# Optimization experiments

Hardware: AMD Instinct MI355X
Metric: run time of the kernel (lower is better)

Reference implementation:

```python
import jax, jax.numpy as jnp
import numpy as np

B, T, C = 2, 2048, 1024
H = 16
D = C // H  # head_dim = 64
SCALE = D ** -0.5


def setup_inputs() -> dict:
    key = jax.random.key(0)
    ks = jax.random.split(key, 5)
    s = 0.02
    return {
        "x": jax.random.normal(ks[0], (B, T, C), dtype=jnp.float32),
        "w_qkv": jax.random.normal(ks[1], (C, 3 * C), dtype=jnp.float32) * s,
        "b_qkv": jnp.zeros((3 * C,), dtype=jnp.float32),
        "w_proj": jax.random.normal(ks[2], (C, C), dtype=jnp.float32) * s,
        "b_proj": jnp.zeros((C,), dtype=jnp.float32),
    }


def reference(x, w_qkv, b_qkv, w_proj, b_proj):
    Bx, Tx, Cx = x.shape
    qkv = x @ w_qkv + b_qkv                      # [B,T,3C]
    q, k, v = jnp.split(qkv, 3, axis=-1)
    # [B,T,C] -> [B,H,T,D]
    q = q.reshape(Bx, Tx, H, D).transpose(0, 2, 1, 3)
    k = k.reshape(Bx, Tx, H, D).transpose(0, 2, 1, 3)
    v = v.reshape(Bx, Tx, H, D).transpose(0, 2, 1, 3)
    attn = jnp.einsum('bhqd,bhkd->bhqk', q, k) * SCALE
    causal = jnp.tril(jnp.ones((Tx, Tx), dtype=bool))
    attn = jnp.where(causal[None, None], attn, -jnp.inf)
    attn = jax.nn.softmax(attn, axis=-1)
    out = jnp.einsum('bhqk,bhkd->bhqd', attn, v)  # [B,H,T,D]
    out = out.transpose(0, 2, 1, 3).reshape(Bx, Tx, Cx)
    return out @ w_proj + b_proj
```

## Files before the change

kernel.cpp:

```cpp
#include <hip/hip_runtime.h>
#include <hip/hip_bf16.h>
#include <math.h>

#define T_SEQ 2048
#define NHEAD 16
#define HDIM  64
#define CDIM  1024
#define KDIM  1024
#define SCALE_L2E 0.1803368801111204f

typedef __attribute__((ext_vector_type(8))) short bf16x8;
typedef __attribute__((ext_vector_type(4))) float f32x4;
typedef __attribute__((ext_vector_type(16))) float f32x16;
typedef __attribute__((ext_vector_type(8))) unsigned short u16x8;
typedef __attribute__((ext_vector_type(4))) unsigned int u32x4;

__device__ __forceinline__ unsigned short f2bf(float f) {
    unsigned int u = __builtin_bit_cast(unsigned int, f);
    u += 0x7fffu + ((u >> 16) & 1u);
    return (unsigned short)(u >> 16);
}
__device__ __forceinline__ unsigned int cvt_pk_bf16(float lo, float hi_) {
    unsigned int r;
    asm("v_cvt_pk_bf16_f32 %0, %1, %2" : "=v"(r) : "v"(lo), "v"(hi_));
    return r;
}
__device__ __forceinline__ void pl32swap(unsigned int &a, unsigned int &b) {
    asm("v_permlane32_swap_b32 %0, %1" : "+v"(a), "+v"(b));
}
__device__ __forceinline__ void gld16(const unsigned short* g, unsigned short* l) {
    __builtin_amdgcn_global_load_lds(
        (const __attribute__((address_space(1))) unsigned int*)g,
        (__attribute__((address_space(3))) unsigned int*)l,
        16, 0, 0);
}

__global__ __launch_bounds__(256) void prep_x(const float* __restrict__ x,
                                              unsigned short* __restrict__ Xb) {
    size_t i = ((size_t)blockIdx.x * 256 + threadIdx.x) * 8;
    float4 a = *(const float4*)(x + i);
    float4 b = *(const float4*)(x + i + 4);
    u32x4 o;
    o[0] = cvt_pk_bf16(a.x, a.y);
    o[1] = cvt_pk_bf16(a.z, a.w);
    o[2] = cvt_pk_bf16(b.x, b.y);
    o[3] = cvt_pk_bf16(b.z, b.w);
    *(u32x4*)(Xb + i) = o;
}

template<int NC>
__global__ __launch_bounds__(256) void prep_w(const float* __restrict__ W,
                                              unsigned short* __restrict__ Wt) {
    __shared__ unsigned short Ls[64][72];
    const int n0 = blockIdx.x * 64, k0 = blockIdx.y * 64;
    const int t = threadIdx.x;
    {
        int kr = t >> 2, nc = (t & 3) * 16;
        #pragma unroll
        for (int j = 0; j < 4; j++) {
            float4 v = *(const float4*)(W + (size_t)(k0 + kr) * NC + n0 + nc + j * 4);
            Ls[nc + j*4 + 0][kr] = f2bf(v.x);
            Ls[nc + j*4 + 1][kr] = f2bf(v.y);
            Ls[nc + j*4 + 2][kr] = f2bf(v.z);
            Ls[nc + j*4 + 3][kr] = f2bf(v.w);
        }
    }
    __syncthreads();
    {
        int nr = t >> 2, kc = (t & 3) * 16;
        u16x8 o0 = *(const u16x8*)&Ls[nr][kc];
        u16x8 o1 = *(const u16x8*)&Ls[nr][kc + 8];
        *(u16x8*)(Wt + (size_t)(n0 + nr) * KDIM + k0 + kc)     = o0;
        *(u16x8*)(Wt + (size_t)(n0 + nr) * KDIM + k0 + kc + 8) = o1;
    }
}

template<int NC, int EPI>
__global__ __launch_bounds__(256) void gemm_k(
    const unsigned short* __restrict__ A, const unsigned short* __restrict__ Wt,
    const float* __restrict__ bias, float* __restrict__ Of,
    unsigned short* __restrict__ Qb, unsigned short* __restrict__ Kb,
    unsigned short* __restrict__ Vt)
{
    __shared__ unsigned short As[128 * 64];
    __shared__ unsigned short Bs[128 * 64];

    const int tid  = threadIdx.x;
    const int lane = tid & 63;
    const int wid  = tid >> 6;
    const int m0 = blockIdx.x * 128;
    const int n0 = blockIdx.y * 128;
    const int wm = (wid >> 1) * 64;
    const int wn = (wid & 1) * 64;
    const int rl = lane & 15;

    const int r8 = lane >> 3, s8 = lane & 7;
    const int swzs = (s8 ^ r8) * 8;

    f32x4 acc[4][4] = {};

    for (int k0 = 0; k0 < KDIM; k0 += 64) {
        #pragma unroll
        for (int c = 0; c < 4; c++) {
            int row = (wid << 5) + (c << 3) + r8;
            gld16(A  + (size_t)(m0 + row) * KDIM + k0 + swzs, &As[(size_t)((wid<<5)+(c<<3)) * 64]);
            gld16(Wt + (size_t)(n0 + row) * KDIM + k0 + swzs, &Bs[(size_t)((wid<<5)+(c<<3)) * 64]);
        }
        __syncthreads();
        #pragma unroll
        for (int kc = 0; kc < 2; kc++) {
            const int sb = kc * 4 + (lane >> 4);
            bf16x8 af[4], bfr[4];
            #pragma unroll
            for (int f = 0; f < 4; f++) {
                int sw = (sb ^ (rl & 7)) * 8;
                af[f]  = *(const bf16x8*)&As[(wm + f*16 + rl) * 64 + sw];
                bfr[f] = *(const bf16x8*)&Bs[(wn + f*16 + rl) * 64 + sw];
            }
            __builtin_amdgcn_s_setprio(1);
            #pragma unroll
            for (int i = 0; i < 4; i++)
                #pragma unroll
                for (int j = 0; j < 4; j++)
                    acc[i][j] = __builtin_amdgcn_mfma_f32_16x16x32_bf16(af[i], bfr[j], acc[i][j], 0, 0, 0);
            __builtin_amdgcn_s_setprio(0);
        }
        __syncthreads();
    }

    #pragma unroll
    for (int j = 0; j < 4; j++) {
        int gn = n0 + wn + j*16 + rl;
        float bv = bias[gn];
        #pragma unroll
        for (int i = 0; i < 4; i++) {
            int gm0 = m0 + wm + i*16 + (lane >> 4) * 4;
            #pragma unroll
            for (int r = 0; r < 4; r++) {
                float v = acc[i][j][r] + bv;
                int gm = gm0 + r;
                if (EPI == 0) {
                    int which = gn >> 10;
                    int cw = gn & 1023;
                    int h = cw >> 6, d = cw & 63;
                    int b = gm >> 11, t = gm & 2047;
                    size_t bh = (size_t)(b * NHEAD + h);
                    if (which == 0)      Qb[(bh * T_SEQ + t) * HDIM + d] = f2bf(v * SCALE_L2E);
                    else if (which == 1) Kb[(bh * T_SEQ + t) * HDIM + d] = f2bf(v);
                    else                 Vt[(bh * HDIM + d) * T_SEQ + t] = f2bf(v);
                } else {
                    Of[(size_t)gm * NC + gn] = v;
                }
            }
        }
    }
}

__global__ __launch_bounds__(128, 4) void attn_k(
    const unsigned short* __restrict__ Qb, const unsigned short* __restrict__ Kb,
    const unsigned short* __restrict__ Vt, unsigned short* __restrict__ AO)
{
    __shared__ unsigned short sbuf[2 * 4096];

    const int tid  = threadIdx.x;
    const int lane = tid & 63;
    const int w    = tid >> 6;
    const int bh   = blockIdx.x;
    const int qt   = 63 - blockIdx.y;
    const int ql   = lane & 31;
    const int hi   = lane >> 5;
    const int qg   = (qt << 5) + ql;

    const unsigned short* Qp = Qb + (size_t)bh * T_SEQ * HDIM;
    const unsigned short* Kp = Kb + (size_t)bh * T_SEQ * HDIM;
    const unsigned short* Vp = Vt + (size_t)bh * HDIM * T_SEQ;

    unsigned short* kbuf = sbuf + w * 4096;
    const char* kbB = (const char*)kbuf;
    const char* vbB = (const char*)(kbuf + 2048);

    const int r8 = lane >> 3, s8 = lane & 7;
    const int r4 = lane >> 2, s4 = lane & 3;
    const unsigned short* kSrc = Kp + (size_t)r8 * HDIM + ((s8 ^ r8) << 3);
    const unsigned short* vSrc = Vp + (size_t)r4 * T_SEQ + ((s4 ^ (r4 & 3)) << 3);

    auto issue_tile = [&](int t) {
        #pragma unroll
        for (int c = 0; c < 4; c++)
            gld16(kSrc + ((size_t)t << 11) + (c << 9), kbuf + (c << 9));
        #pragma unroll
        for (int c = 0; c < 4; c++)
            gld16(vSrc + ((size_t)c << 15) + (t << 5), kbuf + 2048 + (c << 9));
    };

    bf16x8 qf[4];
    #pragma unroll
    for (int dc = 0; dc < 4; dc++)
        qf[dc] = *(const bf16x8*)(Qp + (size_t)qg * HDIM + dc*16 + hi*8);

    float m_run = -INFINITY, l_run = 0.f;
    f32x16 o0 = {}, o1 = {};

    if (w <= qt) {
        issue_tile(w);
        for (int t = w; t <= qt; t += 2) {
            asm volatile("s_waitcnt vmcnt(0)" ::: "memory");
            __builtin_amdgcn_sched_barrier(0);

            bf16x8 kf[4];
            #pragma unroll
            for (int dc = 0; dc < 4; dc++)
                kf[dc] = *(const bf16x8*)(kbB + ql*128 + (((dc << 1 | hi) ^ (ql & 7)) << 4));
            bf16x8 v00 = *(const bf16x8*)(vbB + ql*64        + (((0 | hi) ^ (ql & 3)) << 4));
            bf16x8 v01 = *(const bf16x8*)(vbB + ql*64        + (((2 | hi) ^ (ql & 3)) << 4));
            bf16x8 v10 = *(const bf16x8*)(vbB + (32+ql)*64   + (((0 | hi) ^ (ql & 3)) << 4));
            bf16x8 v11 = *(const bf16x8*)(vbB + (32+ql)*64   + (((2 | hi) ^ (ql & 3)) << 4));
            asm volatile("s_waitcnt lgkmcnt(0)" ::: "memory");
            __builtin_amdgcn_sched_barrier(0);

            if (t + 2 <= qt) issue_tile(t + 2);

            f32x16 s = {};
            __builtin_amdgcn_s_setprio(1);
            #pragma unroll
            for (int dc = 0; dc < 4; dc++)
                s = __builtin_amdgcn_mfma_f32_32x32x16_bf16(kf[dc], qf[dc], s, 0, 0, 0);
            __builtin_amdgcn_s_setprio(0);

            float p[16];
            #pragma unroll
            for (int r = 0; r < 16; r++) p[r] = s[r];
            if (t == qt) {
                #pragma unroll
                for (int r = 0; r < 16; r++) {
                    int kv = (t << 5) + (r & 3) + 8 * (r >> 2) + 4 * hi;
                    p[r] = (kv > qg) ? -INFINITY : p[r];
                }
            }
            float tm = p[0];
            #pragma unroll
            for (int r = 1; r < 16; r++) tm = fmaxf(tm, p[r]);
            tm = fmaxf(tm, __shfl_xor(tm, 32));
            if (__any(tm > m_run + 11.5f)) {
                float mn = fmaxf(m_run, tm);
                float sf = exp2f(m_run - mn);
                m_run = mn;
                l_run *= sf;
                #pragma unroll
                for (int r = 0; r < 16; r++) { o0[r] *= sf; o1[r] *= sf; }
            }
            float rs = 0.f;
            #pragma unroll
            for (int r = 0; r < 16; r++) { p[r] = exp2f(p[r] - m_run); rs += p[r]; }
            rs += __shfl_xor(rs, 32);
            l_run += rs;

            unsigned int c[8];
            #pragma unroll
            for (int i = 0; i < 8; i++) c[i] = cvt_pk_bf16(p[2*i], p[2*i+1]);
            pl32swap(c[0], c[2]);  pl32swap(c[1], c[3]);
            pl32swap(c[4], c[6]);  pl32swap(c[5], c[7]);
            u32x4 b0 = {c[0], c[1], c[2], c[3]};
            u32x4 b1 = {c[4], c[5], c[6], c[7]};
            bf16x8 pf0 = __builtin_bit_cast(bf16x8, b0);
            bf16x8 pf1 = __builtin_bit_cast(bf16x8, b1);

            __builtin_amdgcn_s_setprio(1);
            o0 = __builtin_amdgcn_mfma_f32_32x32x16_bf16(v00, pf0, o0, 0, 0, 0);
            o0 = __builtin_amdgcn_mfma_f32_32x32x16_bf16(v01, pf1, o0, 0, 0, 0);
            o1 = __builtin_amdgcn_mfma_f32_32x32x16_bf16(v10, pf0, o1, 0, 0, 0);
            o1 = __builtin_amdgcn_mfma_f32_32x32x16_bf16(v11, pf1, o1, 0, 0, 0);
            __builtin_amdgcn_s_setprio(0);
        }
    }

    __syncthreads();
    float* lf = (float*)sbuf;
    if (w == 1) {
        #pragma unroll
        for (int j = 0; j < 4; j++) {
            f32x4 a = { o0[4*j], o0[4*j+1], o0[4*j+2], o0[4*j+3] };
            *(f32x4*)(lf + (size_t)(j*64 + lane) * 4) = a;
        }
        #pragma unroll
        for (int j = 0; j < 4; j++) {
            f32x4 a = { o1[4*j], o1[4*j+1], o1[4*j+2], o1[4*j+3] };
            *(f32x4*)(lf + (size_t)((4+j)*64 + lane) * 4) = a;
        }
        lf[2048 + lane*2]     = m_run;
        lf[2048 + lane*2 + 1] = l_run;
    }
    __syncthreads();
    if (w == 0) {
        float m1 = lf[2048 + lane*2], l1 = lf[2048 + lane*2 + 1];
        float m  = fmaxf(m_run, m1);
        float sc0 = exp2f(m_run - m), sc1 = exp2f(m1 - m);
        float linv = 1.f / (l_run * sc0 + l1 * sc1);
        float a0 = sc0 * linv, a1 = sc1 * linv;
        const int b = bh >> 4, h = bh & 15;
        unsigned short* aop = AO + ((size_t)(b * T_SEQ + qg)) * CDIM + h * HDIM;
        #pragma unroll
        for (int qd = 0; qd < 4; qd++) {
            f32x4 x0 = *(const f32x4*)(lf + (size_t)(qd*64 + lane) * 4);
            f32x4 x1 = *(const f32x4*)(lf + (size_t)((4+qd)*64 + lane) * 4);
            uint2 w0, w1;
            w0.x = cvt_pk_bf16(o0[4*qd+0]*a0 + x0[0]*a1, o0[4*qd+1]*a0 + x0[1]*a1);
            w0.y = cvt_pk_bf16(o0[4*qd+2]*a0 + x0[2]*a1, o0[4*qd+3]*a0 + x0[3]*a1);
            w1.x = cvt_pk_bf16(o1[4*qd+0]*a0 + x1[0]*a1, o1[4*qd+1]*a0 + x1[1]*a1);
            w1.y = cvt_pk_bf16(o1[4*qd+2]*a0 + x1[2]*a1, o1[4*qd+3]*a0 + x1[3]*a1);
            *(uint2*)(aop + qd*8 + hi*4)      = w0;
            *(uint2*)(aop + 32 + qd*8 + hi*4) = w1;
        }
    }
}

extern "C" void kernel_launch(void* const* d_in, const int* in_sizes, int n_in,
                              void* d_out, int out_size, void* d_ws, size_t ws_size,
                              hipStream_t stream) {
    const float* x      = (const float*)d_in[0];
    const float* w_qkv  = (const float*)d_in[1];
    const float* b_qkv  = (const float*)d_in[2];
    const float* w_proj = (const float*)d_in[3];
    const float* b_proj = (const float*)d_in[4];
    float* out = (float*)d_out;

    const size_t MI = (size_t)1 << 20;
    unsigned short* base = (unsigned short*)d_ws;
    unsigned short* Qb  = base;
    unsigned short* Kb  = base + 4*MI;
    unsigned short* Vt  = base + 8*MI;
    unsigned short* Wqt = base + 12*MI;
    unsigned short* Wpt = base + 15*MI;
    unsigned short* Xb  = base + 16*MI;
    unsigned short* AO  = Xb;

    prep_x<<<dim3(2048), 256, 0, stream>>>(x, Xb);
    prep_w<3072><<<dim3(48, 16), 256, 0, stream>>>(w_qkv, Wqt);
    prep_w<1024><<<dim3(16, 16), 256, 0, stream>>>(w_proj, Wpt);
    gemm_k<3072, 0><<<dim3(32, 24), 256, 0, stream>>>(
        Xb, Wqt, b_qkv, nullptr, Qb, Kb, Vt);
    attn_k<<<dim3(32, 64), 128, 0, stream>>>(Qb, Kb, Vt, AO);
    gemm_k<1024, 1><<<dim3(32, 8), 256, 0, stream>>>(
        AO, Wpt, b_proj, out, nullptr, nullptr, nullptr);
}
```

Measured before the change: 118.8 us.

## Double-buffer GEMM LDS tiles and load attention K/V directly into registers

```diff
diff --git a/kernel.cpp b/kernel.cpp
--- a/kernel.cpp
+++ b/kernel.cpp
@@ -82,8 +82,8 @@
     unsigned short* __restrict__ Qb, unsigned short* __restrict__ Kb,
     unsigned short* __restrict__ Vt)
 {
-    __shared__ unsigned short As[128 * 64];
-    __shared__ unsigned short Bs[128 * 64];
+    __shared__ unsigned short As[2][128 * 64];
+    __shared__ unsigned short Bs[2][128 * 64];
 
     const int tid  = threadIdx.x;
     const int lane = tid & 63;
@@ -97,16 +97,24 @@
     const int r8 = lane >> 3, s8 = lane & 7;
     const int swzs = (s8 ^ r8) * 8;
 
-    f32x4 acc[4][4] = {};
-
-    for (int k0 = 0; k0 < KDIM; k0 += 64) {
+    auto stage = [&](int b, int k0) {
         #pragma unroll
         for (int c = 0; c < 4; c++) {
             int row = (wid << 5) + (c << 3) + r8;
-            gld16(A  + (size_t)(m0 + row) * KDIM + k0 + swzs, &As[(size_t)((wid<<5)+(c<<3)) * 64]);
-            gld16(Wt + (size_t)(n0 + row) * KDIM + k0 + swzs, &Bs[(size_t)((wid<<5)+(c<<3)) * 64]);
-        }
-        __syncthreads();
+            int dst = ((wid << 5) + (c << 3)) * 64;
+            gld16(A  + (size_t)(m0 + row) * KDIM + k0 + swzs, &As[b][dst]);
+            gld16(Wt + (size_t)(n0 + row) * KDIM + k0 + swzs, &Bs[b][dst]);
+        }
+    };
+
+    f32x4 acc[4][4] = {};
+
+    stage(0, 0);
+    __syncthreads();
+
+    for (int ks = 0; ks < 16; ks++) {
+        const int cur = ks & 1;
+        if (ks < 15) stage(cur ^ 1, (ks + 1) << 6);
         #pragma unroll
         for (int kc = 0; kc < 2; kc++) {
             const int sb = kc * 4 + (lane >> 4);
@@ -114,8 +122,8 @@
             #pragma unroll
             for (int f = 0; f < 4; f++) {
                 int sw = (sb ^ (rl & 7)) * 8;
-                af[f]  = *(const bf16x8*)&As[(wm + f*16 + rl) * 64 + sw];
-                bfr[f] = *(const bf16x8*)&Bs[(wn + f*16 + rl) * 64 + sw];
+                af[f]  = *(const bf16x8*)&As[cur][(wm + f*16 + rl) * 64 + sw];
+                bfr[f] = *(const bf16x8*)&Bs[cur][(wn + f*16 + rl) * 64 + sw];
             }
             __builtin_amdgcn_s_setprio(1);
             #pragma unroll
@@ -160,7 +168,7 @@
     const unsigned short* __restrict__ Qb, const unsigned short* __restrict__ Kb,
     const unsigned short* __restrict__ Vt, unsigned short* __restrict__ AO)
 {
-    __shared__ unsigned short sbuf[2 * 4096];
+    __shared__ float lf[2176];
 
     const int tid  = threadIdx.x;
     const int lane = tid & 63;
@@ -175,23 +183,8 @@
     const unsigned short* Kp = Kb + (size_t)bh * T_SEQ * HDIM;
     const unsigned short* Vp = Vt + (size_t)bh * HDIM * T_SEQ;
 
-    unsigned short* kbuf = sbuf + w * 4096;
-    const char* kbB = (const char*)kbuf;
-    const char* vbB = (const char*)(kbuf + 2048);
-
-    const int r8 = lane >> 3, s8 = lane & 7;
-    const int r4 = lane >> 2, s4 = lane & 3;
-    const unsigned short* kSrc = Kp + (size_t)r8 * HDIM + ((s8 ^ r8) << 3);
-    const unsigned short* vSrc = Vp + (size_t)r4 * T_SEQ + ((s4 ^ (r4 & 3)) << 3);
-
-    auto issue_tile = [&](int t) {
-        #pragma unroll
-        for (int c = 0; c < 4; c++)
-            gld16(kSrc + ((size_t)t << 11) + (c << 9), kbuf + (c << 9));
-        #pragma unroll
-        for (int c = 0; c < 4; c++)
-            gld16(vSrc + ((size_t)c << 15) + (t << 5), kbuf + 2048 + (c << 9));
-    };
+    const unsigned short* kB = Kp + (size_t)ql * HDIM + hi * 8;
+    const unsigned short* vB = Vp + (size_t)ql * T_SEQ + hi * 8;
 
     bf16x8 qf[4];
     #pragma unroll
@@ -201,81 +194,83 @@
     float m_run = -INFINITY, l_run = 0.f;
     f32x16 o0 = {}, o1 = {};
 
+#define LOADK(T, DST) { \
+    const unsigned short* kp_ = kB + ((size_t)(T) << 11); \
+    DST[0] = *(const bf16x8*)(kp_);      DST[1] = *(const bf16x8*)(kp_ + 16); \
+    DST[2] = *(const bf16x8*)(kp_ + 32); DST[3] = *(const bf16x8*)(kp_ + 48); }
+
+#define BODY(T, KR) { \
+    const unsigned short* vp_ = vB + ((T) << 5); \
+    bf16x8 v00 = *(const bf16x8*)(vp_); \
+    bf16x8 v01 = *(const bf16x8*)(vp_ + 16); \
+    bf16x8 v10 = *(const bf16x8*)(vp_ + 32 * T_SEQ); \
+    bf16x8 v11 = *(const bf16x8*)(vp_ + 32 * T_SEQ + 16); \
+    f32x16 s = {}; \
+    __builtin_amdgcn_s_setprio(1); \
+    s = __builtin_amdgcn_mfma_f32_32x32x16_bf16(KR[0], qf[0], s, 0, 0, 0); \
+    s = __builtin_amdgcn_mfma_f32_32x32x16_bf16(KR[1], qf[1], s, 0, 0, 0); \
+    s = __builtin_amdgcn_mfma_f32_32x32x16_bf16(KR[2], qf[2], s, 0, 0, 0); \
+    s = __builtin_amdgcn_mfma_f32_32x32x16_bf16(KR[3], qf[3], s, 0, 0, 0); \
+    __builtin_amdgcn_s_setprio(0); \
+    float p[16]; \
+    _Pragma("unroll") \
+    for (int r = 0; r < 16; r++) p[r] = s[r]; \
+    if ((T) == qt) { \
+        _Pragma("unroll") \
+        for (int r = 0; r < 16; r++) { \
+            int kv = ((T) << 5) + (r & 3) + 8 * (r >> 2) + 4 * hi; \
+            p[r] = (kv > qg) ? -INFINITY : p[r]; \
+        } \
+    } \
+    float tm = p[0]; \
+    _Pragma("unroll") \
+    for (int r = 1; r < 16; r++) tm = fmaxf(tm, p[r]); \
+    tm = fmaxf(tm, __shfl_xor(tm, 32)); \
+    if (__any(tm > m_run + 11.5f)) { \
+        float mn = fmaxf(m_run, tm); \
+        float sf = exp2f(m_run - mn); \
+        m_run = mn; \
+        l_run *= sf; \
+        _Pragma("unroll") \
+        for (int r = 0; r < 16; r++) { o0[r] *= sf; o1[r] *= sf; } \
+    } \
+    float rs = 0.f; \
+    _Pragma("unroll") \
+    for (int r = 0; r < 16; r++) { p[r] = exp2f(p[r] - m_run); rs += p[r]; } \
+    rs += __shfl_xor(rs, 32); \
+    l_run += rs; \
+    unsigned int c[8]; \
+    _Pragma("unroll") \
+    for (int i = 0; i < 8; i++) c[i] = cvt_pk_bf16(p[2*i], p[2*i+1]); \
+    pl32swap(c[0], c[2]);  pl32swap(c[1], c[3]); \
+    pl32swap(c[4], c[6]);  pl32swap(c[5], c[7]); \
+    u32x4 b0_ = {c[0], c[1], c[2], c[3]}; \
+    u32x4 b1_ = {c[4], c[5], c[6], c[7]}; \
+    bf16x8 pf0 = __builtin_bit_cast(bf16x8, b0_); \
+    bf16x8 pf1 = __builtin_bit_cast(bf16x8, b1_); \
+    __builtin_amdgcn_s_setprio(1); \
+    o0 = __builtin_amdgcn_mfma_f32_32x32x16_bf16(v00, pf0, o0, 0, 0, 0); \
+    o0 = __builtin_amdgcn_mfma_f32_32x32x16_bf16(v01, pf1, o0, 0, 0, 0); \
+    o1 = __builtin_amdgcn_mfma_f32_32x32x16_bf16(v10, pf0, o1, 0, 0, 0); \
+    o1 = __builtin_amdgcn_mfma_f32_32x32x16_bf16(v11, pf1, o1, 0, 0, 0); \
+    __builtin_amdgcn_s_setprio(0); }
+
     if (w <= qt) {
-        issue_tile(w);
-        for (int t = w; t <= qt; t += 2) {
-            asm volatile("s_waitcnt vmcnt(0)" ::: "memory");
-            __builtin_amdgcn_sched_barrier(0);
-
-            bf16x8 kf[4];
-            #pragma unroll
-            for (int dc = 0; dc < 4; dc++)
-                kf[dc] = *(const bf16x8*)(kbB + ql*128 + (((dc << 1 | hi) ^ (ql & 7)) << 4));
-            bf16x8 v00 = *(const bf16x8*)(vbB + ql*64        + (((0 | hi) ^ (ql & 3)) << 4));
-            bf16x8 v01 = *(const bf16x8*)(vbB + ql*64        + (((2 | hi) ^ (ql & 3)) << 4));
-            bf16x8 v10 = *(const bf16x8*)(vbB + (32+ql)*64   + (((0 | hi) ^ (ql & 3)) << 4));
-            bf16x8 v11 = *(const bf16x8*)(vbB + (32+ql)*64   + (((2 | hi) ^ (ql & 3)) << 4));
-            asm volatile("s_waitcnt lgkmcnt(0)" ::: "memory");
-            __builtin_amdgcn_sched_barrier(0);
-
-            if (t + 2 <= qt) issue_tile(t + 2);
-
-            f32x16 s = {};
-            __builtin_amdgcn_s_setprio(1);
-            #pragma unroll
-            for (int dc = 0; dc < 4; dc++)
-                s = __builtin_amdgcn_mfma_f32_32x32x16_bf16(kf[dc], qf[dc], s, 0, 0, 0);
-            __builtin_amdgcn_s_setprio(0);
-
-            float p[16];
-            #pragma unroll
-            for (int r = 0; r < 16; r++) p[r] = s[r];
-            if (t == qt) {
-                #pragma unroll
-                for (int r = 0; r < 16; r++) {
-                    int kv = (t << 5) + (r & 3) + 8 * (r >> 2) + 4 * hi;
-                    p[r] = (kv > qg) ? -INFINITY : p[r];
-                }
+        bf16x8 ka[4], kb2[4];
+        LOADK(w, ka);
+        for (int t = w; t <= qt; t += 4) {
+            if (t + 2 <= qt) LOADK(t + 2, kb2);
+            BODY(t, ka);
+            if (t + 2 <= qt) {
+                if (t + 4 <= qt) LOADK(t + 4, ka);
+                BODY(t + 2, kb2);
             }
-            float tm = p[0];
-            #pragma unroll
-            for (int r = 1; r < 16; r++) tm = fmaxf(tm, p[r]);
-            tm = fmaxf(tm, __shfl_xor(tm, 32));
-            if (__any(tm > m_run + 11.5f)) {
-                float mn = fmaxf(m_run, tm);
-                float sf = exp2f(m_run - mn);
-                m_run = mn;
-                l_run *= sf;
-                #pragma unroll
-                for (int r = 0; r < 16; r++) { o0[r] *= sf; o1[r] *= sf; }
-            }
-            float rs = 0.f;
-            #pragma unroll
-            for (int r = 0; r < 16; r++) { p[r] = exp2f(p[r] - m_run); rs += p[r]; }
-            rs += __shfl_xor(rs, 32);
-            l_run += rs;
-
-            unsigned int c[8];
-            #pragma unroll
-            for (int i = 0; i < 8; i++) c[i] = cvt_pk_bf16(p[2*i], p[2*i+1]);
-            pl32swap(c[0], c[2]);  pl32swap(c[1], c[3]);
-            pl32swap(c[4], c[6]);  pl32swap(c[5], c[7]);
-            u32x4 b0 = {c[0], c[1], c[2], c[3]};
-            u32x4 b1 = {c[4], c[5], c[6], c[7]};
-            bf16x8 pf0 = __builtin_bit_cast(bf16x8, b0);
-            bf16x8 pf1 = __builtin_bit_cast(bf16x8, b1);
-
-            __builtin_amdgcn_s_setprio(1);
-            o0 = __builtin_amdgcn_mfma_f32_32x32x16_bf16(v00, pf0, o0, 0, 0, 0);
-            o0 = __builtin_amdgcn_mfma_f32_32x32x16_bf16(v01, pf1, o0, 0, 0, 0);
-            o1 = __builtin_amdgcn_mfma_f32_32x32x16_bf16(v10, pf0, o1, 0, 0, 0);
-            o1 = __builtin_amdgcn_mfma_f32_32x32x16_bf16(v11, pf1, o1, 0, 0, 0);
-            __builtin_amdgcn_s_setprio(0);
-        }
-    }
+        }
+    }
+#undef LOADK
+#undef BODY
 
     __syncthreads();
-    float* lf = (float*)sbuf;
     if (w == 1) {
         #pragma unroll
         for (int j = 0; j < 4; j++) {
```

Result: slower. 160.2 us (+34.9%).

## Split attention KV loop across four waves per block instead of two

Applied to the files above, without the earlier changes.

```diff
diff --git a/kernel.cpp b/kernel.cpp
--- a/kernel.cpp
+++ b/kernel.cpp
@@ -156,11 +156,12 @@
     }
 }
 
-__global__ __launch_bounds__(128, 4) void attn_k(
+__global__ __launch_bounds__(256) void attn_k(
     const unsigned short* __restrict__ Qb, const unsigned short* __restrict__ Kb,
     const unsigned short* __restrict__ Vt, unsigned short* __restrict__ AO)
 {
-    __shared__ unsigned short sbuf[2 * 4096];
+    __shared__ unsigned short sbuf[4 * 4096];
+    __shared__ float mlbuf[3 * 128];
 
     const int tid  = threadIdx.x;
     const int lane = tid & 63;
@@ -203,7 +204,7 @@
 
     if (w <= qt) {
         issue_tile(w);
-        for (int t = w; t <= qt; t += 2) {
+        for (int t = w; t <= qt; t += 4) {
             asm volatile("s_waitcnt vmcnt(0)" ::: "memory");
             __builtin_amdgcn_sched_barrier(0);
 
@@ -218,7 +219,7 @@
             asm volatile("s_waitcnt lgkmcnt(0)" ::: "memory");
             __builtin_amdgcn_sched_barrier(0);
 
-            if (t + 2 <= qt) issue_tile(t + 2);
+            if (t + 4 <= qt) issue_tile(t + 4);
 
             f32x16 s = {};
             __builtin_amdgcn_s_setprio(1);
@@ -276,38 +277,54 @@
 
     __syncthreads();
     float* lf = (float*)sbuf;
-    if (w == 1) {
+    if (w > 0) {
+        float* reg = lf + (size_t)(w - 1) * 2048;
         #pragma unroll
         for (int j = 0; j < 4; j++) {
             f32x4 a = { o0[4*j], o0[4*j+1], o0[4*j+2], o0[4*j+3] };
-            *(f32x4*)(lf + (size_t)(j*64 + lane) * 4) = a;
+            *(f32x4*)(reg + (size_t)(j*64 + lane) * 4) = a;
         }
         #pragma unroll
         for (int j = 0; j < 4; j++) {
             f32x4 a = { o1[4*j], o1[4*j+1], o1[4*j+2], o1[4*j+3] };
-            *(f32x4*)(lf + (size_t)((4+j)*64 + lane) * 4) = a;
-        }
-        lf[2048 + lane*2]     = m_run;
-        lf[2048 + lane*2 + 1] = l_run;
+            *(f32x4*)(reg + (size_t)((4+j)*64 + lane) * 4) = a;
+        }
+        mlbuf[(w - 1) * 128 + lane*2]     = m_run;
+        mlbuf[(w - 1) * 128 + lane*2 + 1] = l_run;
     }
     __syncthreads();
     if (w == 0) {
-        float m1 = lf[2048 + lane*2], l1 = lf[2048 + lane*2 + 1];
-        float m  = fmaxf(m_run, m1);
-        float sc0 = exp2f(m_run - m), sc1 = exp2f(m1 - m);
-        float linv = 1.f / (l_run * sc0 + l1 * sc1);
-        float a0 = sc0 * linv, a1 = sc1 * linv;
+        float m1 = mlbuf[lane*2],       l1 = mlbuf[lane*2 + 1];
+        float m2 = mlbuf[128 + lane*2], l2 = mlbuf[128 + lane*2 + 1];
+        float m3 = mlbuf[256 + lane*2], l3 = mlbuf[256 + lane*2 + 1];
+        float m = fmaxf(fmaxf(m_run, m1), fmaxf(m2, m3));
+        float a0 = exp2f(m_run - m), a1 = exp2f(m1 - m);
+        float a2 = exp2f(m2 - m),    a3 = exp2f(m3 - m);
+        float linv = 1.f / (l_run*a0 + l1*a1 + l2*a2 + l3*a3);
+        a0 *= linv; a1 *= linv; a2 *= linv; a3 *= linv;
         const int b = bh >> 4, h = bh & 15;
         unsigned short* aop = AO + ((size_t)(b * T_SEQ + qg)) * CDIM + h * HDIM;
         #pragma unroll
         for (int qd = 0; qd < 4; qd++) {
-            f32x4 x0 = *(const f32x4*)(lf + (size_t)(qd*64 + lane) * 4);
-            f32x4 x1 = *(const f32x4*)(lf + (size_t)((4+qd)*64 + lane) * 4);
+            f32x4 x1a = *(const f32x4*)(lf + (size_t)(qd*64 + lane) * 4);
+            f32x4 x1b = *(const f32x4*)(lf + (size_t)((4+qd)*64 + lane) * 4);
+            f32x4 x2a = *(const f32x4*)(lf + 2048 + (size_t)(qd*64 + lane) * 4);
+            f32x4 x2b = *(const f32x4*)(lf + 2048 + (size_t)((4+qd)*64 + lane) * 4);
+            f32x4 x3a = *(const f32x4*)(lf + 4096 + (size_t)(qd*64 + lane) * 4);
+            f32x4 x3b = *(const f32x4*)(lf + 4096 + (size_t)((4+qd)*64 + lane) * 4);
             uint2 w0, w1;
-            w0.x = cvt_pk_bf16(o0[4*qd+0]*a0 + x0[0]*a1, o0[4*qd+1]*a0 + x0[1]*a1);
-            w0.y = cvt_pk_bf16(o0[4*qd+2]*a0 + x0[2]*a1, o0[4*qd+3]*a0 + x0[3]*a1);
-            w1.x = cvt_pk_bf16(o1[4*qd+0]*a0 + x1[0]*a1, o1[4*qd+1]*a0 + x1[1]*a1);
-            w1.y = cvt_pk_bf16(o1[4*qd+2]*a0 + x1[2]*a1, o1[4*qd+3]*a0 + x1[3]*a1);
+            w0.x = cvt_pk_bf16(
+                o0[4*qd+0]*a0 + x1a[0]*a1 + x2a[0]*a2 + x3a[0]*a3,
+                o0[4*qd+1]*a0 + x1a[1]*a1 + x2a[1]*a2 + x3a[1]*a3);
+            w0.y = cvt_pk_bf16(
+                o0[4*qd+2]*a0 + x1a[2]*a1 + x2a[2]*a2 + x3a[2]*a3,
+                o0[4*qd+3]*a0 + x1a[3]*a1 + x2a[3]*a2 + x3a[3]*a3);
+            w1.x = cvt_pk_bf16(
+                o1[4*qd+0]*a0 + x1b[0]*a1 + x2b[0]*a2 + x3b[0]*a3,
+                o1[4*qd+1]*a0 + x1b[1]*a1 + x2b[1]*a2 + x3b[1]*a3);
+            w1.y = cvt_pk_bf16(
+                o1[4*qd+2]*a0 + x1b[2]*a1 + x2b[2]*a2 + x3b[2]*a3,
+                o1[4*qd+3]*a0 + x1b[3]*a1 + x2b[3]*a2 + x3b[3]*a3);
             *(uint2*)(aop + qd*8 + hi*4)      = w0;
             *(uint2*)(aop + 32 + qd*8 + hi*4) = w1;
         }
@@ -339,7 +356,7 @@
     prep_w<1024><<<dim3(16, 16), 256, 0, stream>>>(w_proj, Wpt);
     gemm_k<3072, 0><<<dim3(32, 24), 256, 0, stream>>>(
         Xb, Wqt, b_qkv, nullptr, Qb, Kb, Vt);
-    attn_k<<<dim3(32, 64), 128, 0, stream>>>(Qb, Kb, Vt, AO);
+    attn_k<<<dim3(32, 64), 256, 0, stream>>>(Qb, Kb, Vt, AO);
     gemm_k<1024, 1><<<dim3(32, 8), 256, 0, stream>>>(
         AO, Wpt, b_proj, out, nullptr, nullptr, nullptr);
 }
```

Result: slower. 125.3 us (+5.5%).
